# Kernel optimization log

Hardware: AMD Instinct MI355X
Metric: run time of the kernel (lower is better)

## Reference

```python
import jax, jax.numpy as jnp
import numpy as np

EPS = 1e-5
B, N, K = 2, 20000, 17      # batch, num points, k+1 neighbors
CIN = 128                   # bn_size * growth_rate
G = 128                     # growth_rate


def index_points(pts, idx):
    # pts: [B, C, N], idx: [B, S, K] -> [B, C, S, K]
    return jnp.take_along_axis(pts[:, :, :, None], idx[:, None, :, :], axis=2)


def conv_bn_relu(x, W, b, gamma, beta, mean, var):
    # 1x1 Conv2d + BatchNorm2d (inference, running stats) + ReLU
    # x: [B, Cin, N, K], W: [Cout, Cin]
    y = jnp.einsum('oc,bcnk->bonk', W, x) + b[None, :, None, None]
    inv = gamma / jnp.sqrt(var + EPS)
    y = y * inv[None, :, None, None] + (beta - mean * inv)[None, :, None, None]
    return jax.nn.relu(y)


def setup_inputs() -> dict:
    key = jax.random.key(0)
    ks = jax.random.split(key, 16)
    feats = jax.random.normal(ks[0], (B, CIN, N), dtype=jnp.float32)
    pts = jax.random.normal(ks[1], (B, 3, N), dtype=jnp.float32)
    knn_idx = jax.random.randint(ks[2], (B, N, K), 0, N, dtype=jnp.int32)
    s = 0.05
    d = {
        'feats': feats, 'pts': pts, 'knn_idx': knn_idx,
        'Wd': jax.random.normal(ks[3], (G, 3), dtype=jnp.float32) * s,
        'bd': jnp.zeros((G,), jnp.float32),
        'gd': jnp.ones((G,), jnp.float32),
        'betad': jnp.zeros((G,), jnp.float32),
        'md': jax.random.normal(ks[4], (G,), dtype=jnp.float32) * 0.01,
        'vd': jax.random.uniform(ks[5], (G,), jnp.float32, 0.5, 1.5),
        'Wf': jax.random.normal(ks[6], (G, CIN), dtype=jnp.float32) * s,
        'bf': jnp.zeros((G,), jnp.float32),
        'gf': jnp.ones((G,), jnp.float32),
        'betaf': jnp.zeros((G,), jnp.float32),
        'mf': jax.random.normal(ks[7], (G,), dtype=jnp.float32) * 0.01,
        'vf': jax.random.uniform(ks[8], (G,), jnp.float32, 0.5, 1.5),
        'Wp': jax.random.normal(ks[9], (G, G), dtype=jnp.float32) * s,
        'bp': jnp.zeros((G,), jnp.float32),
        'gp': jnp.ones((G,), jnp.float32),
        'betap': jnp.zeros((G,), jnp.float32),
        'mp': jax.random.normal(ks[10], (G,), dtype=jnp.float32) * 0.01,
        'vp': jax.random.uniform(ks[11], (G,), jnp.float32, 0.5, 1.5),
    }
    return d


def reference(feats, pts, knn_idx,
              Wd, bd, gd, betad, md, vd,
              Wf, bf, gf, betaf, mf, vf,
              Wp, bp, gp, betap, mp, vp):
    # Point3DConv.forward with precomputed knn_idx
    knn_pts = index_points(pts, knn_idx)                 # [B,3,N,K]
    knn_delta = knn_pts - pts[:, :, :, None]             # [B,3,N,K]
    knn_delta = conv_bn_relu(knn_delta, Wd, bd, gd, betad, md, vd)   # [B,G,N,K]
    knn_feats = index_points(feats, knn_idx)              # [B,CIN,N,K]
    knn_feats = conv_bn_relu(knn_feats, Wf, bf, gf, betaf, mf, vf)   # [B,G,N,K]
    new_feats = knn_delta * knn_feats                     # [B,G,N,K]
    new_feats = conv_bn_relu(new_feats, Wp, bp, gp, betap, mp, vp)   # [B,G,N,K]
    return new_feats.sum(axis=-1)                         # [B,G,N]
```

## Files before the change

### kernel.cpp

```cpp
#include <hip/hip_runtime.h>
#include <hip/hip_bf16.h>
#include <cstdint>
#include <cstddef>

#define NB 2
#define NPT 20000
#define KNN 17
#define CH 128
#define NT16 (NPT/16)
#define NT32 (NPT/32)
#define EPSV 1e-5f

typedef short short8 __attribute__((ext_vector_type(8)));
typedef float f32x4 __attribute__((ext_vector_type(4)));
typedef float f32x2 __attribute__((ext_vector_type(2)));
typedef unsigned short u16;

__device__ __forceinline__ unsigned cvtpk(float lo, float hi) {
    unsigned r;
    asm("v_cvt_pk_bf16_f32 %0, %1, %2" : "=v"(r) : "v"(lo), "v"(hi));
    return r;
}
__device__ __forceinline__ u16 f2bf1(float x) { return (u16)cvtpk(x, x); }
__device__ __forceinline__ f32x2 pk_fma(f32x2 a, f32x2 b, f32x2 c) {
    f32x2 d;
    asm("v_pk_fma_f32 %0, %1, %2, %3" : "=v"(d) : "v"(a), "v"(b), "v"(c));
    return d;
}
__device__ __forceinline__ f32x2 pk_mul(f32x2 a, f32x2 b) {
    f32x2 d;
    asm("v_pk_mul_f32 %0, %1, %2" : "=v"(d) : "v"(a), "v"(b));
    return d;
}
__device__ __forceinline__ f32x2 bfpair(unsigned w) {
    union { unsigned u; float f; } lo, hi;
    lo.u = w << 16; hi.u = w & 0xffff0000u;
    f32x2 r; r[0] = lo.f; r[1] = hi.f; return r;
}
__device__ __forceinline__ short8 packrow_scaled(const float* wrow, float s) {
    float4 w0 = *(const float4*)(wrow);
    float4 w1 = *(const float4*)(wrow + 4);
    uint4 uu;
    uu.x = cvtpk(w0.x*s, w0.y*s); uu.y = cvtpk(w0.z*s, w0.w*s);
    uu.z = cvtpk(w1.x*s, w1.y*s); uu.w = cvtpk(w1.z*s, w1.w*s);
    union { uint4 u; short8 s8; } cv; cv.u = uu; return cv.s8;
}
__device__ __forceinline__ short8 packrow(const float* wrow) {
    return packrow_scaled(wrow, 1.0f);
}
__device__ __forceinline__ void lds_barrier() {
    asm volatile("s_waitcnt lgkmcnt(0)\n\ts_barrier" ::: "memory");
}

__global__ __launch_bounds__(256) void k_feats(
    const float* __restrict__ feats, const float* __restrict__ Wf,
    const float* __restrict__ bfv, const float* __restrict__ gf,
    const float* __restrict__ betaf, const float* __restrict__ mf,
    const float* __restrict__ vf, u16* __restrict__ Fout)
{
    __shared__ u16 A_lds[32][136];
    __shared__ u16 O_lds[32][136];
    const int t  = threadIdx.x;
    const int b  = blockIdx.x / NT32;
    const int n0 = (blockIdx.x % NT32) * 32;

    {
        const int chunk = t & 7;
        const int cbase = t >> 3;
        const float* base = feats + (size_t)b*CH*NPT + n0 + chunk*4;
        #pragma unroll
        for (int it = 0; it < 4; ++it) {
            int c = it*32 + cbase;
            float4 v = *(const float4*)(base + (size_t)c*NPT);
            A_lds[chunk*4+0][c] = f2bf1(v.x);
            A_lds[chunk*4+1][c] = f2bf1(v.y);
            A_lds[chunk*4+2][c] = f2bf1(v.z);
            A_lds[chunk*4+3][c] = f2bf1(v.w);
        }
    }

    const int lane = t & 63, wid = t >> 6;
    const int h = lane >> 4, r16 = lane & 15;
    const int gb = wid * 32;

    short8 bfrag[2][4];
    float sf[2], tf[2];
    #pragma unroll
    for (int T = 0; T < 2; ++T) {
        int g = gb + T*16 + r16;
        #pragma unroll
        for (int s = 0; s < 4; ++s)
            bfrag[T][s] = packrow(Wf + g*CH + s*32 + h*8);
        float inv = gf[g] * rsqrtf(vf[g] + EPSV);
        sf[T] = inv;
        tf[T] = bfv[g]*inv + betaf[g] - mf[g]*inv;
    }
    lds_barrier();

    #pragma unroll
    for (int sub = 0; sub < 2; ++sub) {
        short8 a[4];
        #pragma unroll
        for (int s = 0; s < 4; ++s)
            a[s] = *(const short8*)&A_lds[sub*16 + r16][s*32 + h*8];
        #pragma unroll
        for (int T = 0; T < 2; ++T) {
            f32x4 acc = {0.f, 0.f, 0.f, 0.f};
            #pragma unroll
            for (int s = 0; s < 4; ++s)
                acc = __builtin_amdgcn_mfma_f32_16x16x32_bf16(a[s], bfrag[T][s], acc, 0, 0, 0);
            #pragma unroll
            for (int r = 0; r < 4; ++r) {
                float y = fmaxf(fmaf(sf[T], acc[r], tf[T]), 0.f);
                O_lds[sub*16 + 4*h + r][gb + T*16 + r16] = f2bf1(y);
            }
        }
    }
    lds_barrier();

    {
        const int pp = t >> 3, cc = (t & 7) * 16;
        uint4 v0 = *(const uint4*)&O_lds[pp][cc];
        uint4 v1 = *(const uint4*)&O_lds[pp][cc + 8];
        u16* dst = Fout + ((size_t)b*NPT + n0 + pp)*CH + cc;
        *(uint4*)dst = v0;
        *(uint4*)(dst + 8) = v1;
    }
}

struct Pref { float4 m; uint4 f; };

__global__ __launch_bounds__(256) void k_main(
    const float* __restrict__ pts, const int* __restrict__ knn,
    const u16* __restrict__ F,
    const float* __restrict__ Wd, const float* __restrict__ bd,
    const float* __restrict__ gd, const float* __restrict__ betad,
    const float* __restrict__ md, const float* __restrict__ vd,
    const float* __restrict__ Wp, const float* __restrict__ bp,
    const float* __restrict__ gp, const float* __restrict__ betap,
    const float* __restrict__ mp, const float* __restrict__ vp,
    float* __restrict__ out)
{
    __shared__ u16    Abuf[2][2][16*128];
    __shared__ float4 metaL[KNN][16];

    const int t  = threadIdx.x;
    const int b  = blockIdx.x / NT16;
    const int n0 = (blockIdx.x % NT16) * 16;

    const float* px = pts + (size_t)b*3*NPT;
    const float* py = px + NPT;
    const float* pz = py + NPT;

    {
        const int* krow = knn + ((size_t)b*NPT + n0)*KNN;
        #pragma unroll 1
        for (int e = t; e < KNN*16; e += 256) {
            int k = e >> 4, p = e & 15;
            int nb = krow[p*KNN + k];
            float4 m;
            m.x = px[nb] - px[n0+p];
            m.y = py[nb] - py[n0+p];
            m.z = pz[nb] - pz[n0+p];
            m.w = __int_as_float(nb << 8);
            metaL[k][p] = m;
        }
    }
    lds_barrier();

    const int p_t = t >> 4, j_t = t & 15, c0 = j_t*8;
    const int lane = t & 63, wid = t >> 6;
    const int h = lane >> 4, r16 = lane & 15;
    const int gb = wid * 32;
    const char* FbjB = (const char*)(F + (size_t)b*NPT*CH + c0);

    const int wOff = p_t*128 + (c0 ^ ((p_t&7)*8));
    int rOff[4];
    #pragma unroll
    for (int s = 0; s < 4; ++s)
        rOff[s] = r16*128 + ((s*32 + h*8) ^ ((r16&7)*8));

    auto issueK = [&](int k)->Pref {
        Pref P;
        P.m = metaL[k][p_t];
        P.f = *(const uint4*)(FbjB + __float_as_int(P.m.w));
        return P;
    };

    Pref PA0 = issueK(0), PA1 = issueK(1);
    Pref PB0 = issueK(2), PB1 = issueK(3);

    short8 bfrag[2][4];
    float tpv[2];
    #pragma unroll
    for (int T = 0; T < 2; ++T) {
        int g = gb + T*16 + r16;
        float inv = gp[g] * rsqrtf(vp[g] + EPSV);
        #pragma unroll
        for (int s = 0; s < 4; ++s)
            bfrag[T][s] = packrow_scaled(Wp + g*CH + s*32 + h*8, inv);
        tpv[T] = bp[g]*inv + betap[g] - mp[g]*inv;
    }

    f32x2 wx2[4], wy2[4], wz2[4], t2[4];
    #pragma unroll
    for (int q = 0; q < 4; ++q) {
        const int ca = c0 + 2*q, cb = ca + 1;
        float inva = gd[ca] * rsqrtf(vd[ca] + EPSV);
        float invb = gd[cb] * rsqrtf(vd[cb] + EPSV);
        wx2[q][0] = Wd[ca*3+0]*inva; wx2[q][1] = Wd[cb*3+0]*invb;
        wy2[q][0] = Wd[ca*3+1]*inva; wy2[q][1] = Wd[cb*3+1]*invb;
        wz2[q][0] = Wd[ca*3+2]*inva; wz2[q][1] = Wd[cb*3+2]*invb;
        t2[q][0]  = bd[ca]*inva + betad[ca] - md[ca]*inva;
        t2[q][1]  = bd[cb]*invb + betad[cb] - md[cb]*invb;
    }

    auto stage = [&](u16* plane, const Pref& Pr) {
        const unsigned fw[4] = {Pr.f.x, Pr.f.y, Pr.f.z, Pr.f.w};
        const f32x2 z2 = {0.f, 0.f};
        f32x2 dx2 = {Pr.m.x, Pr.m.x}, dy2 = {Pr.m.y, Pr.m.y}, dz2 = {Pr.m.z, Pr.m.z};
        unsigned pk[4];
        #pragma unroll
        for (int q = 0; q < 4; ++q) {
            f32x2 d = pk_fma(wx2[q], dx2, pk_fma(wy2[q], dy2, pk_fma(wz2[q], dz2, t2[q])));
            d = __builtin_elementwise_max(d, z2);
            f32x2 pr = pk_mul(d, bfpair(fw[q]));
            pk[q] = cvtpk(pr[0], pr[1]);
        }
        uint4 v; v.x = pk[0]; v.y = pk[1]; v.z = pk[2]; v.w = pk[3];
        *(uint4*)(plane + wOff) = v;
    };

    f32x4 facc[2] = {};
    auto mfmaP = [&](const u16* plane) {
        short8 a[4];
        #pragma unroll
        for (int s = 0; s < 4; ++s)
            a[s] = *(const short8*)(plane + rOff[s]);
        #pragma unroll
        for (int T = 0; T < 2; ++T) {
            f32x4 acc = {0.f,0.f,0.f,0.f};
            #pragma unroll
            for (int s = 0; s < 4; ++s)
                acc = __builtin_amdgcn_mfma_f32_16x16x32_bf16(a[s], bfrag[T][s], acc, 0, 0, 0);
            f32x4 nt = {-tpv[T], -tpv[T], -tpv[T], -tpv[T]};
            facc[T] += __builtin_elementwise_max(acc, nt);
        }
    };

    u16* B0 = &Abuf[0][0][0];
    u16* B1 = &Abuf[1][0][0];

    auto chunk = [&](u16* sb, const u16* mb, Pref& S0, Pref& S1, int r0, int r1) {
        stage(sb, S0);
        stage(sb + 2048, S1);
        if (r0 >= 0) S0 = issueK(r0);
        if (r1 >= 0) S1 = issueK(r1);
        mfmaP(mb);
        mfmaP(mb + 2048);
        lds_barrier();
    };

    stage(B0, PA0);
    stage(B0 + 2048, PA1);
    PA0 = issueK(4); PA1 = issueK(5);
    lds_barrier();

    chunk(B1, B0, PB0, PB1,  6,  7);
    chunk(B0, B1, PA0, PA1,  8,  9);
    chunk(B1, B0, PB0, PB1, 10, 11);
    chunk(B0, B1, PA0, PA1, 12, 13);
    chunk(B1, B0, PB0, PB1, 14, 15);
    chunk(B0, B1, PA0, PA1, 16, -1);
    chunk(B1, B0, PB0, PB1, -1, -1);

    stage(B0, PA0);
    mfmaP(B1);
    mfmaP(B1 + 2048);
    lds_barrier();
    mfmaP(B0);

    #pragma unroll
    for (int T = 0; T < 2; ++T) {
        int g = gb + T*16 + r16;
        f32x4 o = facc[T] + (float)KNN * tpv[T];
        *(f32x4*)(out + ((size_t)b*CH + g)*NPT + n0 + 4*h) = o;
    }
}

extern "C" void kernel_launch(void* const* d_in, const int* in_sizes, int n_in,
                              void* d_out, int out_size, void* d_ws, size_t ws_size,
                              hipStream_t stream)
{
    const float* feats = (const float*)d_in[0];
    const float* pts   = (const float*)d_in[1];
    const int*   knn   = (const int*)d_in[2];
    const float* Wd    = (const float*)d_in[3];
    const float* bd    = (const float*)d_in[4];
    const float* gd    = (const float*)d_in[5];
    const float* betad = (const float*)d_in[6];
    const float* md    = (const float*)d_in[7];
    const float* vd    = (const float*)d_in[8];
    const float* Wf    = (const float*)d_in[9];
    const float* bfv   = (const float*)d_in[10];
    const float* gf    = (const float*)d_in[11];
    const float* betaf = (const float*)d_in[12];
    const float* mf    = (const float*)d_in[13];
    const float* vf    = (const float*)d_in[14];
    const float* Wp    = (const float*)d_in[15];
    const float* bp    = (const float*)d_in[16];
    const float* gp    = (const float*)d_in[17];
    const float* betap = (const float*)d_in[18];
    const float* mp    = (const float*)d_in[19];
    const float* vp    = (const float*)d_in[20];
    float* out = (float*)d_out;
    u16* Fws = (u16*)d_ws;

    k_feats<<<dim3(NB * NT32), 256, 0, stream>>>(feats, Wf, bfv, gf, betaf, mf, vf, Fws);
    k_main <<<dim3(NB * NT16), 256, 0, stream>>>(pts, knn, Fws, Wd, bd, gd, betad, md, vd,
                                                 Wp, bp, gp, betap, mp, vp, out);
}
```

Before: 82.45 us.

## Stage all 17 neighbor planes in LDS before a single barrier, then MFMA

Replaces the double-buffered chunk pipeline, which had a barrier after every pair of neighbor planes, with a two-phase schedule. First all 17 neighbor planes are staged into a larger LDS array while six gathers stay in flight. Then one barrier is taken, and the MFMA phase runs with register double-buffered LDS reads. This removes about eight block barriers and keeps more gathers outstanding. In exchange LDS use grows from about 16KB to about 70KB per block, which may lower occupancy, and staging no longer overlaps with MFMA work.

```diff
diff --git a/kernel.cpp b/kernel.cpp
--- a/kernel.cpp
+++ b/kernel.cpp
@@ -141,7 +141,7 @@
     const float* __restrict__ mp, const float* __restrict__ vp,
     float* __restrict__ out)
 {
-    __shared__ u16    Abuf[2][2][16*128];
+    __shared__ u16    Apl[KNN*2048];
     __shared__ float4 metaL[KNN][16];
 
     const int t  = threadIdx.x;
@@ -187,8 +187,8 @@
         return P;
     };
 
-    Pref PA0 = issueK(0), PA1 = issueK(1);
-    Pref PB0 = issueK(2), PB1 = issueK(3);
+    Pref P0 = issueK(0), P1 = issueK(1), P2 = issueK(2),
+         P3 = issueK(3), P4 = issueK(4), P5 = issueK(5);
 
     short8 bfrag[2][4];
     float tpv[2];
@@ -231,12 +231,28 @@
         *(uint4*)(plane + wOff) = v;
     };
 
+    auto stepk = [&](int k, Pref& Pr, int knext) {
+        stage(Apl + k*2048, Pr);
+        if (knext < KNN) Pr = issueK(knext);
+    };
+    stepk( 0, P0,  6); stepk( 1, P1,  7); stepk( 2, P2,  8);
+    stepk( 3, P3,  9); stepk( 4, P4, 10); stepk( 5, P5, 11);
+    stepk( 6, P0, 12); stepk( 7, P1, 13); stepk( 8, P2, 14);
+    stepk( 9, P3, 15); stepk(10, P4, 16); stepk(11, P5, 99);
+    stepk(12, P0, 99); stepk(13, P1, 99); stepk(14, P2, 99);
+    stepk(15, P3, 99); stepk(16, P4, 99);
+
+    lds_barrier();
+
     f32x4 facc[2] = {};
-    auto mfmaP = [&](const u16* plane) {
-        short8 a[4];
+    short8 aA[4], aB[4];
+    auto LDA = [&](short8* a, int k) {
+        const u16* pl = Apl + k*2048;
         #pragma unroll
         for (int s = 0; s < 4; ++s)
-            a[s] = *(const short8*)(plane + rOff[s]);
+            a[s] = *(const short8*)(pl + rOff[s]);
+    };
+    auto MFMA8 = [&](const short8* a) {
         #pragma unroll
         for (int T = 0; T < 2; ++T) {
             f32x4 acc = {0.f,0.f,0.f,0.f};
@@ -248,37 +264,15 @@
         }
     };
 
-    u16* B0 = &Abuf[0][0][0];
-    u16* B1 = &Abuf[1][0][0];
-
-    auto chunk = [&](u16* sb, const u16* mb, Pref& S0, Pref& S1, int r0, int r1) {
-        stage(sb, S0);
-        stage(sb + 2048, S1);
-        if (r0 >= 0) S0 = issueK(r0);
-        if (r1 >= 0) S1 = issueK(r1);
-        mfmaP(mb);
-        mfmaP(mb + 2048);
-        lds_barrier();
-    };
-
-    stage(B0, PA0);
-    stage(B0 + 2048, PA1);
-    PA0 = issueK(4); PA1 = issueK(5);
-    lds_barrier();
-
-    chunk(B1, B0, PB0, PB1,  6,  7);
-    chunk(B0, B1, PA0, PA1,  8,  9);
-    chunk(B1, B0, PB0, PB1, 10, 11);
-    chunk(B0, B1, PA0, PA1, 12, 13);
-    chunk(B1, B0, PB0, PB1, 14, 15);
-    chunk(B0, B1, PA0, PA1, 16, -1);
-    chunk(B1, B0, PB0, PB1, -1, -1);
-
-    stage(B0, PA0);
-    mfmaP(B1);
-    mfmaP(B1 + 2048);
-    lds_barrier();
-    mfmaP(B0);
+    LDA(aA, 0);
+    #pragma unroll
+    for (int i = 0; i < 8; ++i) {
+        LDA(aB, 2*i + 1);
+        MFMA8(aA);
+        LDA(aA, 2*i + 2);
+        MFMA8(aB);
+    }
+    MFMA8(aA);
 
     #pragma unroll
     for (int T = 0; T < 2; ++T) {
```

Result: faster. 75.96 us (-7.9%).
